# Kernel tuning notes

Hardware: AMD Instinct MI355X
Metric: run time of the kernel (lower is better)

Reference implementation:

```python
import jax, jax.numpy as jnp
import numpy as np

B, C_IN, L = 256, 4, 2048
HNODE, GLEN = 256, 24
SIGMA_CONV, SIGMA_NEU = 0.1, 0.1
DROPPROB = 0.5


def setup_inputs() -> dict:
    key = jax.random.key(0)
    ks = jax.random.split(key, 7)
    x = jax.random.normal(ks[0], (B, C_IN, L), dtype=jnp.float32)
    wConv = SIGMA_CONV * jax.random.normal(ks[1], (HNODE, C_IN, GLEN), dtype=jnp.float32)
    wRect = -jax.random.normal(ks[2], (HNODE,), dtype=jnp.float32)
    wHidden = 0.3 * jax.random.normal(ks[3], (2 * HNODE, 2 * HNODE), dtype=jnp.float32)
    wHiddenBias = 0.3 * jax.random.normal(ks[4], (2 * HNODE,), dtype=jnp.float32)
    wNeu = SIGMA_NEU * jax.random.normal(ks[5], (2 * HNODE, 1), dtype=jnp.float32)
    wNeuBias = SIGMA_NEU * jax.random.normal(ks[6], (1,), dtype=jnp.float32)
    return {"x": x, "wConv": wConv, "wRect": wRect, "wHidden": wHidden,
            "wHiddenBias": wHiddenBias, "wNeu": wNeu, "wNeuBias": wNeuBias}


def reference(x, wConv, wRect, wHidden, wHiddenBias, wNeu, wNeuBias):
    # conv1d, stride 1, no padding: [B, HNODE, L-GLEN+1]
    conv = jax.lax.conv_general_dilated(
        x, wConv, window_strides=(1,), padding='VALID',
        dimension_numbers=('NCH', 'OIH', 'NCH'))
    rect = jnp.maximum(conv + wRect[None, :, None], 0.0)  # bias + relu-clamp
    maxPool = jnp.max(rect, axis=2)   # [B, HNODE]
    avgPool = jnp.mean(rect, axis=2)  # [B, HNODE]
    pool = jnp.concatenate([maxPool, avgPool], axis=1)  # [B, 2*HNODE]
    hid = jnp.maximum(pool @ wHidden + wHiddenBias, 0.0)
    out = DROPPROB * (hid @ wNeu) + wNeuBias  # [B, 1]
    return out
```

## Files before the change

kernel.cpp:

```cpp
#include <hip/hip_runtime.h>
#include <stdint.h>

#define CIN   4
#define LEN   2048
#define HN    256
#define GL    24
#define LOUT  2025
#define XP    2080

typedef short  s16x8 __attribute__((ext_vector_type(8)));
typedef float  f32x4 __attribute__((ext_vector_type(4)));

__device__ float g_pool[256 * 512];

static __device__ __forceinline__ uint16_t f2bf(float f) {
    union { float f; uint32_t u; } v; v.f = f;
    uint32_t u = v.u;
    return (uint16_t)((u + 0x7FFFu + ((u >> 16) & 1u)) >> 16);
}

#define SEL4(D, i) \
    ({ uint4 fu_ = {(D)[(i)], (D)[(i)+1], (D)[(i)+2], (D)[(i)+3]}; \
       __builtin_bit_cast(s16x8, fu_); })

static __device__ __forceinline__ void loadW(
    uint32_t (&E)[3][8], uint32_t (&O)[3][8],
    const uint16_t* xs, const uint16_t* xs2, const int (&abase)[3], int j)
{
    #pragma unroll
    for (int ks = 0; ks < 3; ++ks) {
        const uint4 e0 = *(const uint4*)&xs [abase[ks] + 128 * j];
        const uint4 e1 = *(const uint4*)&xs [abase[ks] + 128 * j + 8];
        const uint4 o0 = *(const uint4*)&xs2[abase[ks] + 128 * j];
        const uint4 o1 = *(const uint4*)&xs2[abase[ks] + 128 * j + 8];
        E[ks][0]=e0.x; E[ks][1]=e0.y; E[ks][2]=e0.z; E[ks][3]=e0.w;
        E[ks][4]=e1.x; E[ks][5]=e1.y; E[ks][6]=e1.z; E[ks][7]=e1.w;
        O[ks][0]=o0.x; O[ks][1]=o0.y; O[ks][2]=o0.z; O[ks][3]=o0.w;
        O[ks][4]=o1.x; O[ks][5]=o1.y; O[ks][6]=o1.z; O[ks][7]=o1.w;
    }
}

static __device__ __forceinline__ void procW(
    const uint32_t (&E)[3][8], const uint32_t (&O)[3][8],
    const s16x8 (&bfrag)[2][3], const float (&negb)[2],
    bool tail, int q, float (&rawmax)[2], float (&sums)[2])
{
    const f32x4 fzero = {0.f, 0.f, 0.f, 0.f};
    #pragma unroll
    for (int p = 0; p < 8; ++p) {
        s16x8 a0, a1, a2;
        if ((p & 1) == 0) {
            a0 = SEL4(E[0], p/2); a1 = SEL4(E[1], p/2); a2 = SEL4(E[2], p/2);
        } else {
            a0 = SEL4(O[0], (p-1)/2); a1 = SEL4(O[1], (p-1)/2); a2 = SEL4(O[2], (p-1)/2);
        }
        __builtin_amdgcn_s_setprio(1);
        f32x4 acc0, acc1;
        acc0 = __builtin_amdgcn_mfma_f32_16x16x32_bf16(a0, bfrag[0][0], fzero, 0, 0, 0);
        acc1 = __builtin_amdgcn_mfma_f32_16x16x32_bf16(a0, bfrag[1][0], fzero, 0, 0, 0);
        acc0 = __builtin_amdgcn_mfma_f32_16x16x32_bf16(a1, bfrag[0][1], acc0, 0, 0, 0);
        acc1 = __builtin_amdgcn_mfma_f32_16x16x32_bf16(a1, bfrag[1][1], acc1, 0, 0, 0);
        acc0 = __builtin_amdgcn_mfma_f32_16x16x32_bf16(a2, bfrag[0][2], acc0, 0, 0, 0);
        acc1 = __builtin_amdgcn_mfma_f32_16x16x32_bf16(a2, bfrag[1][2], acc1, 0, 0, 0);
        __builtin_amdgcn_s_setprio(0);

        if (!tail) {
            #pragma unroll
            for (int s = 0; s < 2; ++s) {
                const f32x4 a = (s == 0) ? acc0 : acc1;
                float t0 = fmaxf(a[0], negb[s]), t1 = fmaxf(a[1], negb[s]);
                float t2 = fmaxf(a[2], negb[s]), t3 = fmaxf(a[3], negb[s]);
                sums[s] += (t0 + t1) + (t2 + t3);
                rawmax[s] = fmaxf(fmaxf(rawmax[s], a[0]), a[1]);
                rawmax[s] = fmaxf(fmaxf(rawmax[s], a[2]), a[3]);
            }
        } else {
            #pragma unroll
            for (int s = 0; s < 2; ++s) {
                const f32x4 a = (s == 0) ? acc0 : acc1;
                #pragma unroll
                for (int r = 0; r < 4; ++r) {
                    int tpos = p + 128 * 15 + 32 * q + 8 * r;
                    float t = (tpos < LOUT) ? fmaxf(a[r], negb[s])
                                            : negb[s];
                    sums[s]   += t;
                    rawmax[s]  = fmaxf(rawmax[s], t);
                }
            }
        }
    }
}

__global__ __launch_bounds__(512) __attribute__((amdgpu_waves_per_eu(2, 2)))
void conv_pool_kernel(
    const float* __restrict__ x, const float* __restrict__ wConv,
    const float* __restrict__ wRect)
{
    __shared__ uint16_t xs [CIN * XP + 8];
    __shared__ uint16_t xs2[CIN * XP + 8];

    const int tid  = threadIdx.x;
    const int b    = blockIdx.x;
    const int lane = tid & 63;
    const int wid  = tid >> 6;
    const int n    = lane & 15;
    const int q    = lane >> 4;

    const float* xb = x + (size_t)b * (CIN * LEN);
    #pragma unroll
    for (int it = 0; it < 4; ++it) {
        int i = (tid + it * 512) * 4;
        float4 v = *(const float4*)(xb + i);
        int c = i >> 11, off = i & 2047;
        uint64_t pk =  (uint64_t)f2bf(v.x)
                    | ((uint64_t)f2bf(v.y) << 16)
                    | ((uint64_t)f2bf(v.z) << 32)
                    | ((uint64_t)f2bf(v.w) << 48);
        *(uint64_t*)&xs[c * XP + off] = pk;
    }
    if (tid < 64) {
        int c = tid >> 4, o = (tid & 15) * 2;
        *(uint32_t*)&xs[c * XP + 2048 + o] = 0u;
    }
    if (tid < 4) *(uint32_t*)&xs[CIN * XP + tid * 2] = 0u;

    s16x8 bfrag[2][3];
    float negb[2];
    #pragma unroll
    for (int s = 0; s < 2; ++s) {
        int h = wid * 32 + s * 16 + n;
        negb[s] = -wRect[h];
        #pragma unroll
        for (int ks = 0; ks < 3; ++ks) {
            int jb = ks * 4 + q;
            const float* wp_ = wConv + h * (CIN * GL) + jb * 8;
            float4 w0 = *(const float4*)(wp_);
            float4 w1 = *(const float4*)(wp_ + 4);
            s16x8 f;
            f[0]=(short)f2bf(w0.x); f[1]=(short)f2bf(w0.y);
            f[2]=(short)f2bf(w0.z); f[3]=(short)f2bf(w0.w);
            f[4]=(short)f2bf(w1.x); f[5]=(short)f2bf(w1.y);
            f[6]=(short)f2bf(w1.z); f[7]=(short)f2bf(w1.w);
            bfrag[s][ks] = f;
        }
    }

    int abase[3];
    #pragma unroll
    for (int ks = 0; ks < 3; ++ks) {
        int jb = ks * 4 + q;
        int c = jb / 3, g0 = (jb % 3) * 8;
        abase[ks] = c * XP + g0 + 8 * n;
    }

    __syncthreads();

    {
        const uint32_t* s0 = (const uint32_t*)xs;
        uint32_t*       s1 = (uint32_t*)xs2;
        #pragma unroll 1
        for (int g = tid; g < (CIN * XP) / 8; g += 512) {
            uint4 a = *(const uint4*)&s0[4 * g];
            uint32_t nx = s0[4 * g + 4];
            uint4 r;
            r.x = __builtin_amdgcn_alignbit(a.y, a.x, 16);
            r.y = __builtin_amdgcn_alignbit(a.z, a.y, 16);
            r.z = __builtin_amdgcn_alignbit(a.w, a.z, 16);
            r.w = __builtin_amdgcn_alignbit(nx,  a.w, 16);
            *(uint4*)&s1[4 * g] = r;
        }
    }
    __syncthreads();

    float rawmax[2] = {-1e30f, -1e30f};
    float sums[2]   = {0.f, 0.f};

    uint32_t EA[3][8], OA[3][8], EB[3][8], OB[3][8];
    loadW(EA, OA, xs, xs2, abase, 0);
    #pragma unroll 1
    for (int jj = 0; jj < 16; jj += 2) {
        loadW(EB, OB, xs, xs2, abase, jj + 1);
        procW(EA, OA, bfrag, negb, false, q, rawmax, sums);
        loadW(EA, OA, xs, xs2, abase, (jj + 2 < 16) ? jj + 2 : 15);
        procW(EB, OB, bfrag, negb, (jj + 1 == 15), q, rawmax, sums);
    }

    #pragma unroll
    for (int s = 0; s < 2; ++s) {
        float m  = rawmax[s], sm = sums[s];
        m  = fmaxf(m, __shfl_xor(m, 16, 64));  sm += __shfl_xor(sm, 16, 64);
        m  = fmaxf(m, __shfl_xor(m, 32, 64));  sm += __shfl_xor(sm, 32, 64);
        if (q == 0) {
            int h = wid * 32 + s * 16 + n;
            float bia = -negb[s];
            g_pool[(size_t)b * 512 + h]       = fmaxf(m + bia, 0.f);
            g_pool[(size_t)b * 512 + 256 + h] = (sm + 2048.f * bia) * (1.0f / 2025.0f);
        }
    }
}

__global__ __launch_bounds__(512, 2) void mlp_kernel(
    const float* __restrict__ wH, const float* __restrict__ bH,
    const float* __restrict__ wNeu, const float* __restrict__ wNeuB,
    float* __restrict__ out)
{
    __shared__ float pl[2][512];
    __shared__ float part[8][2];

    const int tid  = threadIdx.x;
    const int bg   = blockIdx.x;
    const int lane = tid & 63;
    const int og   = tid >> 6;
    const int o    = og * 64 + lane;

    if (tid < 256) {
        int i = tid * 4;
        *(float4*)&pl[0][i] = *(const float4*)(g_pool + (size_t)bg * 1024 + i);
    }
    __syncthreads();

    float acc0 = 0.f, acc1 = 0.f;
    const float* prow0 = &pl[0][0];
    const float* prow1 = &pl[1][0];
    #pragma unroll 4
    for (int i = 0; i < 512; i += 4) {
        float4 p0 = *(const float4*)(prow0 + i);
        float4 p1 = *(const float4*)(prow1 + i);
        float w0 = wH[(i + 0) * 512 + o];
        float w1 = wH[(i + 1) * 512 + o];
        float w2 = wH[(i + 2) * 512 + o];
        float w3 = wH[(i + 3) * 512 + o];
        acc0 = fmaf(p0.x, w0, acc0); acc0 = fmaf(p0.y, w1, acc0);
        acc0 = fmaf(p0.z, w2, acc0); acc0 = fmaf(p0.w, w3, acc0);
        acc1 = fmaf(p1.x, w0, acc1); acc1 = fmaf(p1.y, w1, acc1);
        acc1 = fmaf(p1.z, w2, acc1); acc1 = fmaf(p1.w, w3, acc1);
    }
    float hb  = bH[o];
    float wn  = wNeu[o];
    float v0  = fmaxf(acc0 + hb, 0.f) * wn;
    float v1  = fmaxf(acc1 + hb, 0.f) * wn;
    #pragma unroll
    for (int dlt = 1; dlt < 64; dlt <<= 1) {
        v0 += __shfl_xor(v0, dlt, 64);
        v1 += __shfl_xor(v1, dlt, 64);
    }
    if (lane == 0) { part[og][0] = v0; part[og][1] = v1; }
    __syncthreads();

    if (tid < 2) {
        float s = 0.f;
        #pragma unroll
        for (int g = 0; g < 8; ++g) s += part[g][tid];
        out[bg * 2 + tid] = 0.5f * s + wNeuB[0];
    }
}

extern "C" void kernel_launch(void* const* d_in, const int* in_sizes, int n_in,
                              void* d_out, int out_size, void* d_ws, size_t ws_size,
                              hipStream_t stream) {
    const float* x        = (const float*)d_in[0];
    const float* wConv    = (const float*)d_in[1];
    const float* wRect    = (const float*)d_in[2];
    const float* wHidden  = (const float*)d_in[3];
    const float* wHidBias = (const float*)d_in[4];
    const float* wNeu     = (const float*)d_in[5];
    const float* wNeuBias = (const float*)d_in[6];
    float* out  = (float*)d_out;
    (void)d_ws; (void)ws_size;

    conv_pool_kernel<<<256, 512, 0, stream>>>(x, wConv, wRect);
    mlp_kernel<<<128, 512, 0, stream>>>(wHidden, wHidBias, wNeu, wNeuBias, out);
}
```

Baseline: 122.2 us.

## Split conv-pool work per sample across four blocks and merge partials in MLP

Each sample's conv+pool is now split across four 256-thread blocks: two halves of the output positions and two halves of the filters. That gives 1024 blocks instead of 256, so the 256 CUs get better occupancy and tail balance. Each block loads only its half of the input (with halo) into shared memory and writes raw partial max/sum values. The MLP kernel combines the two position halves and applies bias, ReLU and the mean scaling. The explicit register double-buffering of LDS loads is dropped in favour of a simpler loop, which may expose some LDS latency.

```diff
diff --git a/kernel.cpp b/kernel.cpp
--- a/kernel.cpp
+++ b/kernel.cpp
@@ -6,12 +6,12 @@
 #define HN    256
 #define GL    24
 #define LOUT  2025
-#define XP    2080
+#define XPH   1056
 
 typedef short  s16x8 __attribute__((ext_vector_type(8)));
 typedef float  f32x4 __attribute__((ext_vector_type(4)));
 
-__device__ float g_pool[256 * 512];
+__device__ float g_part[256][2][512];
 
 static __device__ __forceinline__ uint16_t f2bf(float f) {
     union { float f; uint32_t u; } v; v.f = f;
@@ -23,112 +23,45 @@
     ({ uint4 fu_ = {(D)[(i)], (D)[(i)+1], (D)[(i)+2], (D)[(i)+3]}; \
        __builtin_bit_cast(s16x8, fu_); })
 
-static __device__ __forceinline__ void loadW(
-    uint32_t (&E)[3][8], uint32_t (&O)[3][8],
-    const uint16_t* xs, const uint16_t* xs2, const int (&abase)[3], int j)
-{
-    #pragma unroll
-    for (int ks = 0; ks < 3; ++ks) {
-        const uint4 e0 = *(const uint4*)&xs [abase[ks] + 128 * j];
-        const uint4 e1 = *(const uint4*)&xs [abase[ks] + 128 * j + 8];
-        const uint4 o0 = *(const uint4*)&xs2[abase[ks] + 128 * j];
-        const uint4 o1 = *(const uint4*)&xs2[abase[ks] + 128 * j + 8];
-        E[ks][0]=e0.x; E[ks][1]=e0.y; E[ks][2]=e0.z; E[ks][3]=e0.w;
-        E[ks][4]=e1.x; E[ks][5]=e1.y; E[ks][6]=e1.z; E[ks][7]=e1.w;
-        O[ks][0]=o0.x; O[ks][1]=o0.y; O[ks][2]=o0.z; O[ks][3]=o0.w;
-        O[ks][4]=o1.x; O[ks][5]=o1.y; O[ks][6]=o1.z; O[ks][7]=o1.w;
-    }
-}
-
-static __device__ __forceinline__ void procW(
-    const uint32_t (&E)[3][8], const uint32_t (&O)[3][8],
-    const s16x8 (&bfrag)[2][3], const float (&negb)[2],
-    bool tail, int q, float (&rawmax)[2], float (&sums)[2])
-{
-    const f32x4 fzero = {0.f, 0.f, 0.f, 0.f};
-    #pragma unroll
-    for (int p = 0; p < 8; ++p) {
-        s16x8 a0, a1, a2;
-        if ((p & 1) == 0) {
-            a0 = SEL4(E[0], p/2); a1 = SEL4(E[1], p/2); a2 = SEL4(E[2], p/2);
-        } else {
-            a0 = SEL4(O[0], (p-1)/2); a1 = SEL4(O[1], (p-1)/2); a2 = SEL4(O[2], (p-1)/2);
-        }
-        __builtin_amdgcn_s_setprio(1);
-        f32x4 acc0, acc1;
-        acc0 = __builtin_amdgcn_mfma_f32_16x16x32_bf16(a0, bfrag[0][0], fzero, 0, 0, 0);
-        acc1 = __builtin_amdgcn_mfma_f32_16x16x32_bf16(a0, bfrag[1][0], fzero, 0, 0, 0);
-        acc0 = __builtin_amdgcn_mfma_f32_16x16x32_bf16(a1, bfrag[0][1], acc0, 0, 0, 0);
-        acc1 = __builtin_amdgcn_mfma_f32_16x16x32_bf16(a1, bfrag[1][1], acc1, 0, 0, 0);
-        acc0 = __builtin_amdgcn_mfma_f32_16x16x32_bf16(a2, bfrag[0][2], acc0, 0, 0, 0);
-        acc1 = __builtin_amdgcn_mfma_f32_16x16x32_bf16(a2, bfrag[1][2], acc1, 0, 0, 0);
-        __builtin_amdgcn_s_setprio(0);
-
-        if (!tail) {
-            #pragma unroll
-            for (int s = 0; s < 2; ++s) {
-                const f32x4 a = (s == 0) ? acc0 : acc1;
-                float t0 = fmaxf(a[0], negb[s]), t1 = fmaxf(a[1], negb[s]);
-                float t2 = fmaxf(a[2], negb[s]), t3 = fmaxf(a[3], negb[s]);
-                sums[s] += (t0 + t1) + (t2 + t3);
-                rawmax[s] = fmaxf(fmaxf(rawmax[s], a[0]), a[1]);
-                rawmax[s] = fmaxf(fmaxf(rawmax[s], a[2]), a[3]);
-            }
-        } else {
-            #pragma unroll
-            for (int s = 0; s < 2; ++s) {
-                const f32x4 a = (s == 0) ? acc0 : acc1;
-                #pragma unroll
-                for (int r = 0; r < 4; ++r) {
-                    int tpos = p + 128 * 15 + 32 * q + 8 * r;
-                    float t = (tpos < LOUT) ? fmaxf(a[r], negb[s])
-                                            : negb[s];
-                    sums[s]   += t;
-                    rawmax[s]  = fmaxf(rawmax[s], t);
-                }
-            }
-        }
-    }
-}
-
-__global__ __launch_bounds__(512) __attribute__((amdgpu_waves_per_eu(2, 2)))
+__global__ __launch_bounds__(256) __attribute__((amdgpu_waves_per_eu(3, 4)))
 void conv_pool_kernel(
     const float* __restrict__ x, const float* __restrict__ wConv,
     const float* __restrict__ wRect)
 {
-    __shared__ uint16_t xs [CIN * XP + 8];
-    __shared__ uint16_t xs2[CIN * XP + 8];
+    __shared__ uint16_t xs [CIN * XPH + 8];
+    __shared__ uint16_t xs2[CIN * XPH + 8];
 
     const int tid  = threadIdx.x;
-    const int b    = blockIdx.x;
+    const int b    = blockIdx.x >> 2;
+    const int nh   = (blockIdx.x >> 1) & 1;
+    const int wh   = blockIdx.x & 1;
     const int lane = tid & 63;
     const int wid  = tid >> 6;
     const int n    = lane & 15;
     const int q    = lane >> 4;
 
     const float* xb = x + (size_t)b * (CIN * LEN);
-    #pragma unroll
-    for (int it = 0; it < 4; ++it) {
-        int i = (tid + it * 512) * 4;
-        float4 v = *(const float4*)(xb + i);
-        int c = i >> 11, off = i & 2047;
-        uint64_t pk =  (uint64_t)f2bf(v.x)
-                    | ((uint64_t)f2bf(v.y) << 16)
-                    | ((uint64_t)f2bf(v.z) << 32)
-                    | ((uint64_t)f2bf(v.w) << 48);
-        *(uint64_t*)&xs[c * XP + off] = pk;
-    }
-    if (tid < 64) {
-        int c = tid >> 4, o = (tid & 15) * 2;
-        *(uint32_t*)&xs[c * XP + 2048 + o] = 0u;
-    }
-    if (tid < 4) *(uint32_t*)&xs[CIN * XP + tid * 2] = 0u;
+    for (int f = tid; f < CIN * (XPH / 4); f += 256) {
+        int c  = f / (XPH / 4);
+        int k4 = (f - c * (XPH / 4)) * 4;
+        int p0 = wh * 1024 + k4;
+        uint64_t pk = 0;
+        if (p0 < LEN) {
+            float4 v = *(const float4*)(xb + c * LEN + p0);
+            pk =  (uint64_t)f2bf(v.x)
+               | ((uint64_t)f2bf(v.y) << 16)
+               | ((uint64_t)f2bf(v.z) << 32)
+               | ((uint64_t)f2bf(v.w) << 48);
+        }
+        *(uint64_t*)&xs[c * XPH + k4] = pk;
+    }
+    if (tid < 4) *(uint32_t*)&xs[CIN * XPH + tid * 2] = 0u;
 
     s16x8 bfrag[2][3];
     float negb[2];
     #pragma unroll
     for (int s = 0; s < 2; ++s) {
-        int h = wid * 32 + s * 16 + n;
+        int h = nh * 128 + wid * 32 + s * 16 + n;
         negb[s] = -wRect[h];
         #pragma unroll
         for (int ks = 0; ks < 3; ++ks) {
@@ -150,7 +83,7 @@
     for (int ks = 0; ks < 3; ++ks) {
         int jb = ks * 4 + q;
         int c = jb / 3, g0 = (jb % 3) * 8;
-        abase[ks] = c * XP + g0 + 8 * n;
+        abase[ks] = c * XPH + g0 + 8 * n;
     }
 
     __syncthreads();
@@ -159,7 +92,7 @@
         const uint32_t* s0 = (const uint32_t*)xs;
         uint32_t*       s1 = (uint32_t*)xs2;
         #pragma unroll 1
-        for (int g = tid; g < (CIN * XP) / 8; g += 512) {
+        for (int g = tid; g < (CIN * XPH) / 8; g += 256) {
             uint4 a = *(const uint4*)&s0[4 * g];
             uint32_t nx = s0[4 * g + 4];
             uint4 r;
@@ -174,15 +107,68 @@
 
     float rawmax[2] = {-1e30f, -1e30f};
     float sums[2]   = {0.f, 0.f};
-
-    uint32_t EA[3][8], OA[3][8], EB[3][8], OB[3][8];
-    loadW(EA, OA, xs, xs2, abase, 0);
+    const f32x4 fzero = {0.f, 0.f, 0.f, 0.f};
+
     #pragma unroll 1
-    for (int jj = 0; jj < 16; jj += 2) {
-        loadW(EB, OB, xs, xs2, abase, jj + 1);
-        procW(EA, OA, bfrag, negb, false, q, rawmax, sums);
-        loadW(EA, OA, xs, xs2, abase, (jj + 2 < 16) ? jj + 2 : 15);
-        procW(EB, OB, bfrag, negb, (jj + 1 == 15), q, rawmax, sums);
+    for (int jl = 0; jl < 8; ++jl) {
+        const bool tail = (wh == 1) && (jl == 7);
+
+        uint32_t E[3][8], O[3][8];
+        #pragma unroll
+        for (int ks = 0; ks < 3; ++ks) {
+            const uint4 e0 = *(const uint4*)&xs [abase[ks] + 128 * jl];
+            const uint4 e1 = *(const uint4*)&xs [abase[ks] + 128 * jl + 8];
+            const uint4 o0 = *(const uint4*)&xs2[abase[ks] + 128 * jl];
+            const uint4 o1 = *(const uint4*)&xs2[abase[ks] + 128 * jl + 8];
+            E[ks][0]=e0.x; E[ks][1]=e0.y; E[ks][2]=e0.z; E[ks][3]=e0.w;
+            E[ks][4]=e1.x; E[ks][5]=e1.y; E[ks][6]=e1.z; E[ks][7]=e1.w;
+            O[ks][0]=o0.x; O[ks][1]=o0.y; O[ks][2]=o0.z; O[ks][3]=o0.w;
+            O[ks][4]=o1.x; O[ks][5]=o1.y; O[ks][6]=o1.z; O[ks][7]=o1.w;
+        }
+
+        #pragma unroll
+        for (int p = 0; p < 8; ++p) {
+            s16x8 a0, a1, a2;
+            if ((p & 1) == 0) {
+                a0 = SEL4(E[0], p/2); a1 = SEL4(E[1], p/2); a2 = SEL4(E[2], p/2);
+            } else {
+                a0 = SEL4(O[0], (p-1)/2); a1 = SEL4(O[1], (p-1)/2); a2 = SEL4(O[2], (p-1)/2);
+            }
+            __builtin_amdgcn_s_setprio(1);
+            f32x4 acc0, acc1;
+            acc0 = __builtin_amdgcn_mfma_f32_16x16x32_bf16(a0, bfrag[0][0], fzero, 0, 0, 0);
+            acc1 = __builtin_amdgcn_mfma_f32_16x16x32_bf16(a0, bfrag[1][0], fzero, 0, 0, 0);
+            acc0 = __builtin_amdgcn_mfma_f32_16x16x32_bf16(a1, bfrag[0][1], acc0, 0, 0, 0);
+            acc1 = __builtin_amdgcn_mfma_f32_16x16x32_bf16(a1, bfrag[1][1], acc1, 0, 0, 0);
+            acc0 = __builtin_amdgcn_mfma_f32_16x16x32_bf16(a2, bfrag[0][2], acc0, 0, 0, 0);
+            acc1 = __builtin_amdgcn_mfma_f32_16x16x32_bf16(a2, bfrag[1][2], acc1, 0, 0, 0);
+            __builtin_amdgcn_s_setprio(0);
+
+            if (!tail) {
+                #pragma unroll
+                for (int s = 0; s < 2; ++s) {
+                    const f32x4 a = (s == 0) ? acc0 : acc1;
+                    float t0 = fmaxf(a[0], negb[s]), t1 = fmaxf(a[1], negb[s]);
+                    float t2 = fmaxf(a[2], negb[s]), t3 = fmaxf(a[3], negb[s]);
+                    sums[s] += (t0 + t1) + (t2 + t3);
+                    rawmax[s] = fmaxf(fmaxf(rawmax[s], a[0]), a[1]);
+                    rawmax[s] = fmaxf(fmaxf(rawmax[s], a[2]), a[3]);
+                }
+            } else {
+                #pragma unroll
+                for (int s = 0; s < 2; ++s) {
+                    const f32x4 a = (s == 0) ? acc0 : acc1;
+                    #pragma unroll
+                    for (int r = 0; r < 4; ++r) {
+                        int tpos = p + 128 * 15 + 32 * q + 8 * r;
+                        float t = (tpos < LOUT) ? fmaxf(a[r], negb[s])
+                                                : negb[s];
+                        sums[s]   += t;
+                        rawmax[s]  = fmaxf(rawmax[s], t);
+                    }
+                }
+            }
+        }
     }
 
     #pragma unroll
@@ -191,18 +177,17 @@
         m  = fmaxf(m, __shfl_xor(m, 16, 64));  sm += __shfl_xor(sm, 16, 64);
         m  = fmaxf(m, __shfl_xor(m, 32, 64));  sm += __shfl_xor(sm, 32, 64);
         if (q == 0) {
-            int h = wid * 32 + s * 16 + n;
-            float bia = -negb[s];
-            g_pool[(size_t)b * 512 + h]       = fmaxf(m + bia, 0.f);
-            g_pool[(size_t)b * 512 + 256 + h] = (sm + 2048.f * bia) * (1.0f / 2025.0f);
+            int h = nh * 128 + wid * 32 + s * 16 + n;
+            g_part[b][wh][h]       = m;
+            g_part[b][wh][256 + h] = sm;
         }
     }
 }
 
 __global__ __launch_bounds__(512, 2) void mlp_kernel(
-    const float* __restrict__ wH, const float* __restrict__ bH,
-    const float* __restrict__ wNeu, const float* __restrict__ wNeuB,
-    float* __restrict__ out)
+    const float* __restrict__ wRect, const float* __restrict__ wH,
+    const float* __restrict__ bH, const float* __restrict__ wNeu,
+    const float* __restrict__ wNeuB, float* __restrict__ out)
 {
     __shared__ float pl[2][512];
     __shared__ float part[8][2];
@@ -214,8 +199,27 @@
     const int o    = og * 64 + lane;
 
     if (tid < 256) {
-        int i = tid * 4;
-        *(float4*)&pl[0][i] = *(const float4*)(g_pool + (size_t)bg * 1024 + i);
+        int i   = tid * 4;
+        int smp = i >> 9;
+        int c   = i & 511;
+        const int bb = bg * 2 + smp;
+        float4 v0 = *(const float4*)&g_part[bb][0][c];
+        float4 v1 = *(const float4*)&g_part[bb][1][c];
+        float4 r;
+        if (c < 256) {
+            float4 wr = *(const float4*)(wRect + c);
+            r.x = fmaxf(fmaxf(v0.x, v1.x) + wr.x, 0.f);
+            r.y = fmaxf(fmaxf(v0.y, v1.y) + wr.y, 0.f);
+            r.z = fmaxf(fmaxf(v0.z, v1.z) + wr.z, 0.f);
+            r.w = fmaxf(fmaxf(v0.w, v1.w) + wr.w, 0.f);
+        } else {
+            float4 wr = *(const float4*)(wRect + c - 256);
+            r.x = (v0.x + v1.x + 2048.f * wr.x) * (1.0f / 2025.0f);
+            r.y = (v0.y + v1.y + 2048.f * wr.y) * (1.0f / 2025.0f);
+            r.z = (v0.z + v1.z + 2048.f * wr.z) * (1.0f / 2025.0f);
+            r.w = (v0.w + v1.w + 2048.f * wr.w) * (1.0f / 2025.0f);
+        }
+        *(float4*)&pl[0][i] = r;
     }
     __syncthreads();
 
@@ -268,6 +272,6 @@
     float* out  = (float*)d_out;
     (void)d_ws; (void)ws_size;
 
-    conv_pool_kernel<<<256, 512, 0, stream>>>(x, wConv, wRect);
-    mlp_kernel<<<128, 512, 0, stream>>>(wHidden, wHidBias, wNeu, wNeuBias, out);
-}
+    conv_pool_kernel<<<1024, 256, 0, stream>>>(x, wConv, wRect);
+    mlp_kernel<<<128, 512, 0, stream>>>(wRect, wHidden, wHidBias, wNeu, wNeuBias, out);
+}
```

Measured after the change: 123.1 us. Within noise of the previous version (+0.7%).
